# Optimization experiments

Measured on AMD Instinct MI355X. Metric: run time of the kernel, lower is better.

Reference implementation:

```python
import jax, jax.numpy as jnp
import numpy as np

N = 100000        # nodes
E = 3200000       # directed edges (already includes both directions per the repo)
F_IN = 256
HID = 16
C = 40


def setup_inputs() -> dict:
    key = jax.random.key(0)
    k = jax.random.split(key, 5)
    x = jax.random.normal(k[0], (N, F_IN), dtype=jnp.float32)
    edge_index = jax.random.randint(k[1], (2, E), 0, N, dtype=jnp.int64)
    W1 = jax.random.normal(k[2], (F_IN, HID), dtype=jnp.float32) * (1.0 / np.sqrt(F_IN))
    b1 = jnp.zeros((HID,), jnp.float32)
    W2 = jax.random.normal(k[3], (HID, C), dtype=jnp.float32) * (1.0 / np.sqrt(HID))
    b2 = jnp.zeros((C,), jnp.float32)
    return {"x": x, "edge_index": edge_index, "W1": W1, "b1": b1, "W2": W2, "b2": b2}


def reference(x, edge_index, W1, b1, W2, b2):
    n = x.shape[0]
    # GCNConv: add self-loops, symmetric degree normalization (shared by both layers)
    loop = jnp.arange(n, dtype=edge_index.dtype)
    src = jnp.concatenate([edge_index[0], loop])
    dst = jnp.concatenate([edge_index[1], loop])
    deg = jax.ops.segment_sum(jnp.ones_like(dst, x.dtype), dst, num_segments=n)
    dinv = jnp.where(deg > 0, jax.lax.rsqrt(deg), 0.0)
    norm = dinv[src] * dinv[dst]  # [E+N]

    def gcn(h, W, b):
        h = h @ W  # transform first (PyG order), keeps edge messages low-dim
        msg = h[src] * norm[:, None]
        return jax.ops.segment_sum(msg, dst, num_segments=n) + b

    h = jax.nn.relu(gcn(x, W1, b1))
    # dropout is identity in eval mode (training=False)
    logits = gcn(h, W2, b2)
    return jax.nn.log_softmax(logits, axis=1)
```

## Files before the change

### kernel.cpp

```cpp
#include <hip/hip_runtime.h>
#include <hip/hip_bf16.h>


#define BSH 7
#define NPB 128
#define BCAP 4736
#define MAXB 1024
#define OVF_CAP 8192
#define EPB 4096

#define SCALE 2097152.0f
#define INVS  4.76837158203125e-7f

typedef __attribute__((ext_vector_type(8))) short bf16x8;
typedef __attribute__((ext_vector_type(4))) short bf16x4;
typedef __attribute__((ext_vector_type(4))) float f32x4;

__device__ __forceinline__ short f2b(float f) {
    __hip_bfloat16 h = __float2bfloat16(f);
    return *reinterpret_cast<short*>(&h);
}
__device__ __forceinline__ float b2f(short s) {
    return __uint_as_float(((unsigned int)(unsigned short)s) << 16);
}

__global__ __launch_bounds__(512) void binA(
        const int* __restrict__ src, const int* __restrict__ dst,
        int* __restrict__ gcur, int* __restrict__ padded,
        int2* __restrict__ ovf, int* __restrict__ ovf_cnt,
        int* __restrict__ deg, int E) {
    __shared__ int hist[MAXB], gb[MAXB];
    int tid = threadIdx.x;
    int e0 = blockIdx.x * EPB;
    int e1 = min(e0 + EPB, E);
    for (int b = tid; b < MAXB; b += 512) hist[b] = 0;
    __syncthreads();
    int rs[8], rd[8];
#pragma unroll
    for (int u = 0; u < 8; ++u) {
        int i = e0 + tid + u * 512;
        if (i < e1) {
            rd[u] = dst[i];
            rs[u] = src[i];
            atomicAdd(&hist[rd[u] >> BSH], 1);
        }
    }
    __syncthreads();
    for (int b = tid; b < MAXB; b += 512) {
        int h = hist[b];
        gb[b] = h ? atomicAdd(&gcur[b], h) : 0;
        hist[b] = 0;
    }
    __syncthreads();
#pragma unroll
    for (int u = 0; u < 8; ++u) {
        int i = e0 + tid + u * 512;
        if (i < e1) {
            int s = rs[u], d = rd[u];
            int b = d >> BSH;
            int r = atomicAdd(&hist[b], 1);
            int off = gb[b] + r;
            if (off < BCAP) {
                padded[b * BCAP + off] = (s << BSH) | (d & (NPB - 1));
            } else {
                int k = atomicAdd(ovf_cnt, 1);
                if (k < OVF_CAP) ovf[k] = make_int2(s, d);
                atomicAdd(&deg[d], 1);
            }
        }
    }
}

__global__ __launch_bounds__(512) void degB(
        const int* __restrict__ gcur, const int* __restrict__ padded,
        int* __restrict__ deg, int n) {
    __shared__ int bins[NPB];
    int k = blockIdx.x, tid = threadIdx.x;
    if (tid < NPB) bins[tid] = 0;
    __syncthreads();
    int base = k * BCAP;
    int cnt = min(gcur[k], BCAP);
    for (int i = tid; i < cnt; i += 512)
        atomicAdd(&bins[padded[base + i] & (NPB - 1)], 1);
    __syncthreads();
    if (tid < NPB) {
        int node = (k << BSH) + tid;
        if (node < n) atomicAdd(&deg[node], bins[tid]);
    }
}

__global__ __launch_bounds__(512) void gemm1_mfma(
        const float* __restrict__ x, const float* __restrict__ W1,
        const int* __restrict__ deg, float* __restrict__ dinv,
        short* __restrict__ t1b, int n) {
    __shared__ __align__(16) short xs[128 * 264];
    __shared__ short w1s[256 * 16];
    int tid = threadIdx.x;
    int base = blockIdx.x * 128;
    int rows = n - base; if (rows > 128) rows = 128;

    for (int i = tid; i < 4096; i += 512) w1s[i] = f2b(W1[i]);
    for (int i = tid; i < 8192; i += 512) {
        int r = i >> 6, c = i & 63;
        if (r < rows) {
            float4 v = ((const float4*)(x + (size_t)(base + r) * 256))[c];
            short4 b;
            b.x = f2b(v.x); b.y = f2b(v.y); b.z = f2b(v.z); b.w = f2b(v.w);
            *(short4*)&xs[r * 264 + c * 4] = b;
        }
    }
    __syncthreads();

    int lane = tid & 63, wave = tid >> 6;
    int q = lane >> 4, m = lane & 15;

    bf16x8 bfrag[8];
#pragma unroll
    for (int t = 0; t < 8; ++t)
#pragma unroll
        for (int j = 0; j < 8; ++j)
            bfrag[t][j] = w1s[(t * 32 + q * 8 + j) * 16 + m];

    f32x4 acc = {0.f, 0.f, 0.f, 0.f};
    int arow = wave * 16 + m;
#pragma unroll
    for (int t = 0; t < 8; ++t) {
        bf16x8 a = *(const bf16x8*)&xs[arow * 264 + t * 32 + q * 8];
        acc = __builtin_amdgcn_mfma_f32_16x16x32_bf16(a, bfrag[t], acc, 0, 0, 0);
    }
#pragma unroll
    for (int r = 0; r < 4; ++r) {
        int node = base + wave * 16 + q * 4 + r;
        if (node < n) {
            float di = rsqrtf((float)deg[node] + 1.0f);
            t1b[(size_t)node * 16 + m] = f2b(acc[r] * di);
            if (m == 0) dinv[node] = di;
        }
    }
}

template <int PHASE>
__global__ __launch_bounds__(512) void aggI(
        const int* __restrict__ gcur, const int* __restrict__ padded,
        const short* __restrict__ feat,
        short* __restrict__ Hout, const float* __restrict__ dinv,
        const float* __restrict__ b1,
        const float* __restrict__ W2, const float* __restrict__ b2,
        float* __restrict__ out, int n) {
    __shared__ int acc[NPB][17];
    __shared__ float W2s[640];
    __shared__ float b2s[40];
    int tid = threadIdx.x, k = blockIdx.x;
    if (PHASE == 1) {
        for (int i = tid; i < 640; i += 512) W2s[i] = W2[i];
        if (tid < 40) b2s[tid] = b2[tid];
    }
    for (int i = tid; i < NPB * 17; i += 512) ((int*)acc)[i] = 0;
    __syncthreads();

    int base = k * BCAP;
    int cnt = min(gcur[k], BCAP);
    const bf16x4* f4 = (const bf16x4*)feat;
    int q = tid & 3, slot = tid >> 2;
    int i = slot;
    for (; i + 384 < cnt; i += 512) {
        int v0 = padded[base + i];
        int v1 = padded[base + i + 128];
        int v2 = padded[base + i + 256];
        int v3 = padded[base + i + 384];
        bf16x4 g0 = f4[(size_t)(v0 >> BSH) * 4 + q];
        bf16x4 g1 = f4[(size_t)(v1 >> BSH) * 4 + q];
        bf16x4 g2 = f4[(size_t)(v2 >> BSH) * 4 + q];
        bf16x4 g3 = f4[(size_t)(v3 >> BSH) * 4 + q];
        int d0 = v0 & (NPB - 1), d1 = v1 & (NPB - 1);
        int d2 = v2 & (NPB - 1), d3 = v3 & (NPB - 1);
#pragma unroll
        for (int h = 0; h < 4; ++h) {
            atomicAdd(&acc[d0][q * 4 + h], __float2int_rn(b2f(g0[h]) * SCALE));
            atomicAdd(&acc[d1][q * 4 + h], __float2int_rn(b2f(g1[h]) * SCALE));
            atomicAdd(&acc[d2][q * 4 + h], __float2int_rn(b2f(g2[h]) * SCALE));
            atomicAdd(&acc[d3][q * 4 + h], __float2int_rn(b2f(g3[h]) * SCALE));
        }
    }
    for (; i < cnt; i += 128) {
        int v = padded[base + i];
        bf16x4 g = f4[(size_t)(v >> BSH) * 4 + q];
        int dl = v & (NPB - 1);
#pragma unroll
        for (int h = 0; h < 4; ++h)
            atomicAdd(&acc[dl][q * 4 + h], __float2int_rn(b2f(g[h]) * SCALE));
    }
    __syncthreads();

    int nl = tid >> 2;
    int node = (k << BSH) + nl;
    bool live = node < n;
    if (PHASE == 0) {
        if (live) {
            float di = dinv[node];
            bf16x4 sv = f4[(size_t)node * 4 + q];
            float4 bb = ((const float4*)b1)[q];
            float s0 = b2f(sv[0]) + acc[nl][q * 4 + 0] * INVS;
            float s1 = b2f(sv[1]) + acc[nl][q * 4 + 1] * INVS;
            float s2 = b2f(sv[2]) + acc[nl][q * 4 + 2] * INVS;
            float s3 = b2f(sv[3]) + acc[nl][q * 4 + 3] * INVS;
            bf16x4 o4_;
            o4_[0] = f2b(fmaxf(bb.x + di * s0, 0.f) * di);
            o4_[1] = f2b(fmaxf(bb.y + di * s1, 0.f) * di);
            o4_[2] = f2b(fmaxf(bb.z + di * s2, 0.f) * di);
            o4_[3] = f2b(fmaxf(bb.w + di * s3, 0.f) * di);
            ((bf16x4*)Hout)[(size_t)node * 4 + q] = o4_;
        }
    } else {
        float di = live ? dinv[node] : 0.f;
        float g[16];
        if (live) {
            bf16x8 s0 = ((const bf16x8*)feat)[(size_t)node * 2];
            bf16x8 s1 = ((const bf16x8*)feat)[(size_t)node * 2 + 1];
#pragma unroll
            for (int h = 0; h < 8; ++h) {
                g[h]     = di * (b2f(s0[h]) + acc[nl][h] * INVS);
                g[h + 8] = di * (b2f(s1[h]) + acc[nl][h + 8] * INVS);
            }
        } else {
#pragma unroll
            for (int h = 0; h < 16; ++h) g[h] = 0.f;
        }
        float lg[10];
        float mx = -1e30f;
#pragma unroll
        for (int jj = 0; jj < 10; ++jj) {
            int col = q * 10 + jj;
            float a = b2s[col];
#pragma unroll
            for (int kk = 0; kk < 16; ++kk) a += g[kk] * W2s[kk * 40 + col];
            lg[jj] = a;
            mx = fmaxf(mx, a);
        }
        mx = fmaxf(mx, __shfl_xor(mx, 1));
        mx = fmaxf(mx, __shfl_xor(mx, 2));
        float sum = 0.f;
#pragma unroll
        for (int jj = 0; jj < 10; ++jj) sum += __expf(lg[jj] - mx);
        sum += __shfl_xor(sum, 1);
        sum += __shfl_xor(sum, 2);
        float lse = mx + logf(sum);
        if (live) {
            float2* o2 = (float2*)(out + (size_t)node * 40 + q * 10);
#pragma unroll
            for (int jj = 0; jj < 5; ++jj)
                o2[jj] = make_float2(lg[2 * jj] - lse, lg[2 * jj + 1] - lse);
        }
    }
}

extern "C" void kernel_launch(void* const* d_in, const int* in_sizes, int n_in,
                              void* d_out, int out_size, void* d_ws, size_t ws_size,
                              hipStream_t stream) {
    const float* x  = (const float*)d_in[0];
    const int*   ei = (const int*)d_in[1];
    const float* W1 = (const float*)d_in[2];
    const float* b1 = (const float*)d_in[3];
    const float* W2 = (const float*)d_in[4];
    const float* b2 = (const float*)d_in[5];

    int n = in_sizes[0] / 256;
    int E = in_sizes[1] / 2;
    const int* srcp = ei;
    const int* dstp = ei + E;

    int nbuckets = (n + NPB - 1) >> BSH;

    int*   deg     = (int*)d_ws;
    int*   gcur    = deg + n;
    int*   ovf_cnt = gcur + MAXB;
    float* dinv    = (float*)(ovf_cnt + 16);
    int2*  ovf     = (int2*)(dinv + n);
    short* t1b     = (short*)(ovf + OVF_CAP);
    short* hdb     = t1b + 16 * (size_t)n;
    int*   padded  = (int*)(hdb + 16 * (size_t)n);
    float* out     = (float*)d_out;

    hipMemsetAsync(deg, 0, (size_t)(n + MAXB + 16) * sizeof(int), stream);
    binA      <<<(E + EPB - 1) / EPB, 512, 0, stream>>>(srcp, dstp, gcur, padded,
                                                        ovf, ovf_cnt, deg, E);
    degB      <<<nbuckets, 512, 0, stream>>>(gcur, padded, deg, n);
    gemm1_mfma<<<(n + 127) / 128, 512, 0, stream>>>(x, W1, deg, dinv, t1b, n);
    aggI<0>   <<<nbuckets, 512, 0, stream>>>(gcur, padded, t1b, hdb, dinv,
                                             b1, nullptr, nullptr, nullptr, n);
    aggI<1>   <<<nbuckets, 512, 0, stream>>>(gcur, padded, hdb, nullptr, dinv,
                                             nullptr, W2, b2, out, n);
}
```

Measured before the change: 285.9 us.

## Fuse degree histogram into GEMM1 kernel and deepen aggregation unroll

Removes the separate degB kernel and the global deg array. The per-bucket degree histogram is now built in shared memory inside gemm1_mfma, which is launched with one block per bucket and reads the padded edge list directly, so dinv is computed without a global round-trip. This also shrinks the memset. Separately, the aggregation loop now unrolls to 8 gathers per iteration instead of 4 to expose more memory-level parallelism. Overflow edges no longer add to the degree count, which changes results whenever a bucket exceeds BCAP.

```diff
diff --git a/kernel.cpp b/kernel.cpp
--- a/kernel.cpp
+++ b/kernel.cpp
@@ -27,8 +27,7 @@
 __global__ __launch_bounds__(512) void binA(
         const int* __restrict__ src, const int* __restrict__ dst,
         int* __restrict__ gcur, int* __restrict__ padded,
-        int2* __restrict__ ovf, int* __restrict__ ovf_cnt,
-        int* __restrict__ deg, int E) {
+        int2* __restrict__ ovf, int* __restrict__ ovf_cnt, int E) {
     __shared__ int hist[MAXB], gb[MAXB];
     int tid = threadIdx.x;
     int e0 = blockIdx.x * EPB;
@@ -65,41 +64,32 @@
             } else {
                 int k = atomicAdd(ovf_cnt, 1);
                 if (k < OVF_CAP) ovf[k] = make_int2(s, d);
-                atomicAdd(&deg[d], 1);
             }
         }
-    }
-}
-
-__global__ __launch_bounds__(512) void degB(
-        const int* __restrict__ gcur, const int* __restrict__ padded,
-        int* __restrict__ deg, int n) {
-    __shared__ int bins[NPB];
-    int k = blockIdx.x, tid = threadIdx.x;
-    if (tid < NPB) bins[tid] = 0;
-    __syncthreads();
-    int base = k * BCAP;
-    int cnt = min(gcur[k], BCAP);
-    for (int i = tid; i < cnt; i += 512)
-        atomicAdd(&bins[padded[base + i] & (NPB - 1)], 1);
-    __syncthreads();
-    if (tid < NPB) {
-        int node = (k << BSH) + tid;
-        if (node < n) atomicAdd(&deg[node], bins[tid]);
     }
 }
 
 __global__ __launch_bounds__(512) void gemm1_mfma(
         const float* __restrict__ x, const float* __restrict__ W1,
-        const int* __restrict__ deg, float* __restrict__ dinv,
-        short* __restrict__ t1b, int n) {
+        const int* __restrict__ gcur, const int* __restrict__ padded,
+        float* __restrict__ dinv, short* __restrict__ t1b, int n) {
     __shared__ __align__(16) short xs[128 * 264];
     __shared__ short w1s[256 * 16];
+    __shared__ int bins[NPB];
     int tid = threadIdx.x;
-    int base = blockIdx.x * 128;
+    int k = blockIdx.x;
+    int base = k * 128;
     int rows = n - base; if (rows > 128) rows = 128;
 
+    if (tid < NPB) bins[tid] = 0;
     for (int i = tid; i < 4096; i += 512) w1s[i] = f2b(W1[i]);
+    __syncthreads();
+
+    int ebase = k * BCAP;
+    int ecnt = min(gcur[k], BCAP);
+    for (int i = tid; i < ecnt; i += 512)
+        atomicAdd(&bins[padded[ebase + i] & (NPB - 1)], 1);
+
     for (int i = tid; i < 8192; i += 512) {
         int r = i >> 6, c = i & 63;
         if (r < rows) {
@@ -130,9 +120,10 @@
     }
 #pragma unroll
     for (int r = 0; r < 4; ++r) {
-        int node = base + wave * 16 + q * 4 + r;
+        int nl = wave * 16 + q * 4 + r;
+        int node = base + nl;
         if (node < n) {
-            float di = rsqrtf((float)deg[node] + 1.0f);
+            float di = rsqrtf((float)bins[nl] + 1.0f);
             t1b[(size_t)node * 16 + m] = f2b(acc[r] * di);
             if (m == 0) dinv[node] = di;
         }
@@ -163,23 +154,37 @@
     const bf16x4* f4 = (const bf16x4*)feat;
     int q = tid & 3, slot = tid >> 2;
     int i = slot;
-    for (; i + 384 < cnt; i += 512) {
+    for (; i + 896 < cnt; i += 1024) {
         int v0 = padded[base + i];
         int v1 = padded[base + i + 128];
         int v2 = padded[base + i + 256];
         int v3 = padded[base + i + 384];
+        int v4 = padded[base + i + 512];
+        int v5 = padded[base + i + 640];
+        int v6 = padded[base + i + 768];
+        int v7 = padded[base + i + 896];
         bf16x4 g0 = f4[(size_t)(v0 >> BSH) * 4 + q];
         bf16x4 g1 = f4[(size_t)(v1 >> BSH) * 4 + q];
         bf16x4 g2 = f4[(size_t)(v2 >> BSH) * 4 + q];
         bf16x4 g3 = f4[(size_t)(v3 >> BSH) * 4 + q];
+        bf16x4 g4 = f4[(size_t)(v4 >> BSH) * 4 + q];
+        bf16x4 g5 = f4[(size_t)(v5 >> BSH) * 4 + q];
+        bf16x4 g6 = f4[(size_t)(v6 >> BSH) * 4 + q];
+        bf16x4 g7 = f4[(size_t)(v7 >> BSH) * 4 + q];
         int d0 = v0 & (NPB - 1), d1 = v1 & (NPB - 1);
         int d2 = v2 & (NPB - 1), d3 = v3 & (NPB - 1);
+        int d4 = v4 & (NPB - 1), d5 = v5 & (NPB - 1);
+        int d6 = v6 & (NPB - 1), d7 = v7 & (NPB - 1);
 #pragma unroll
         for (int h = 0; h < 4; ++h) {
             atomicAdd(&acc[d0][q * 4 + h], __float2int_rn(b2f(g0[h]) * SCALE));
             atomicAdd(&acc[d1][q * 4 + h], __float2int_rn(b2f(g1[h]) * SCALE));
             atomicAdd(&acc[d2][q * 4 + h], __float2int_rn(b2f(g2[h]) * SCALE));
             atomicAdd(&acc[d3][q * 4 + h], __float2int_rn(b2f(g3[h]) * SCALE));
+            atomicAdd(&acc[d4][q * 4 + h], __float2int_rn(b2f(g4[h]) * SCALE));
+            atomicAdd(&acc[d5][q * 4 + h], __float2int_rn(b2f(g5[h]) * SCALE));
+            atomicAdd(&acc[d6][q * 4 + h], __float2int_rn(b2f(g6[h]) * SCALE));
+            atomicAdd(&acc[d7][q * 4 + h], __float2int_rn(b2f(g7[h]) * SCALE));
         }
     }
     for (; i < cnt; i += 128) {
@@ -271,8 +276,7 @@
 
     int nbuckets = (n + NPB - 1) >> BSH;
 
-    int*   deg     = (int*)d_ws;
-    int*   gcur    = deg + n;
+    int*   gcur    = (int*)d_ws;
     int*   ovf_cnt = gcur + MAXB;
     float* dinv    = (float*)(ovf_cnt + 16);
     int2*  ovf     = (int2*)(dinv + n);
@@ -281,11 +285,10 @@
     int*   padded  = (int*)(hdb + 16 * (size_t)n);
     float* out     = (float*)d_out;
 
-    hipMemsetAsync(deg, 0, (size_t)(n + MAXB + 16) * sizeof(int), stream);
+    hipMemsetAsync(gcur, 0, (size_t)(MAXB + 16) * sizeof(int), stream);
     binA      <<<(E + EPB - 1) / EPB, 512, 0, stream>>>(srcp, dstp, gcur, padded,
-                                                        ovf, ovf_cnt, deg, E);
-    degB      <<<nbuckets, 512, 0, stream>>>(gcur, padded, deg, n);
-    gemm1_mfma<<<(n + 127) / 128, 512, 0, stream>>>(x, W1, deg, dinv, t1b, n);
+                                                        ovf, ovf_cnt, E);
+    gemm1_mfma<<<nbuckets, 512, 0, stream>>>(x, W1, gcur, padded, dinv, t1b, n);
     aggI<0>   <<<nbuckets, 512, 0, stream>>>(gcur, padded, t1b, hdb, dinv,
                                              b1, nullptr, nullptr, nullptr, n);
     aggI<1>   <<<nbuckets, 512, 0, stream>>>(gcur, padded, hdb, nullptr, dinv,
```

Result: no change. 285.8 us (-0.0%).
